# Kernel optimization log

Hardware: AMD Instinct MI355X
Metric: run time of the kernel (lower is better)

Reference implementation:

```python
import jax, jax.numpy as jnp
import numpy as np

B, N, D, S, H, ITERS = 128, 4096, 64, 7, 128, 3
EPS = 1e-8
LN_EPS = 1e-5


def _ln(x, g, b):
    mu = jnp.mean(x, axis=-1, keepdims=True)
    var = jnp.mean(jnp.square(x - mu), axis=-1, keepdims=True)
    return (x - mu) * jax.lax.rsqrt(var + LN_EPS) * g + b


def setup_inputs() -> dict:
    key = jax.random.key(0)
    ks = jax.random.split(key, 20)
    xav = lambda k, shp: jax.random.normal(k, shp, jnp.float32) * (2.0 / sum(shp[-2:])) ** 0.5
    inp = {
        "inputs": jax.random.normal(ks[0], (B, N, D), jnp.float32),
        "noise_bg": jax.random.normal(ks[1], (B, 1, D), jnp.float32),
        "noise_fg": jax.random.normal(ks[2], (B, S - 1, D), jnp.float32),
        "ln_in_g": jnp.ones((D,), jnp.float32), "ln_in_b": jnp.zeros((D,), jnp.float32),
        "ln_slot_g": jnp.ones((D,), jnp.float32), "ln_slot_b": jnp.zeros((D,), jnp.float32),
        "ln_mlp_g": jnp.ones((D,), jnp.float32), "ln_mlp_b": jnp.zeros((D,), jnp.float32),
        "Wq": xav(ks[3], (D, D)), "Wk": xav(ks[4], (D, D)), "Wv": xav(ks[5], (D, D)),
        "W_ih": xav(ks[6], (3 * D, D)), "W_hh": xav(ks[7], (3 * D, D)),
        "b_ih": jnp.zeros((3 * D,), jnp.float32), "b_hh": jnp.zeros((3 * D,), jnp.float32),
        "mlp_w1": xav(ks[8], (H, D)), "mlp_b1": jnp.zeros((H,), jnp.float32),
        "mlp_w2": xav(ks[9], (D, H)), "mlp_b2": jnp.zeros((D,), jnp.float32),
        "slots_bg_mu": xav(ks[10], (1, 1, D)),
        "slots_bg_log_sigma": xav(ks[11], (1, 1, D)),
        "slots_mu": xav(ks[12], (1, 1, D)),
        "slots_log_sigma": xav(ks[13], (1, 1, D)),
    }
    return inp


def _gru(x, h, W_ih, W_hh, b_ih, b_hh):
    # x, h: [M, D]; PyTorch GRUCell math, gate order r, z, n
    gi = x @ W_ih.T + b_ih
    gh = h @ W_hh.T + b_hh
    i_r, i_z, i_n = jnp.split(gi, 3, axis=-1)
    h_r, h_z, h_n = jnp.split(gh, 3, axis=-1)
    r = jax.nn.sigmoid(i_r + h_r)
    z = jax.nn.sigmoid(i_z + h_z)
    n = jnp.tanh(i_n + r * h_n)
    return (1.0 - z) * n + z * h


def reference(inputs, noise_bg, noise_fg, ln_in_g, ln_in_b, ln_slot_g, ln_slot_b,
              ln_mlp_g, ln_mlp_b, Wq, Wk, Wv, W_ih, W_hh, b_ih, b_hh,
              mlp_w1, mlp_b1, mlp_w2, mlp_b2,
              slots_bg_mu, slots_bg_log_sigma, slots_mu, slots_log_sigma):
    x = _ln(inputs, ln_in_g, ln_in_b)          # [B, N, D]
    k = jnp.einsum('bnd,ed->bne', x, Wk)       # [B, N, D]
    v = jnp.einsum('bnd,ed->bne', x, Wv)

    bg = slots_bg_mu + jnp.exp(slots_bg_log_sigma) * noise_bg   # [B, 1, D]
    fg = slots_mu + jnp.exp(slots_log_sigma) * noise_fg          # [B, S-1, D]
    slots = jnp.concatenate([bg, fg], axis=1)                    # [B, S, D]

    scale = D ** (-0.5)
    for _ in range(ITERS):
        slots_prev = slots
        s = _ln(slots, ln_slot_g, ln_slot_b)
        q = jnp.einsum('bsd,ed->bse', s, Wq)                     # [B, S, D]
        logits = scale * jnp.einsum('bnd,bsd->bns', k, q)        # [B, N, S]
        attn = jax.nn.softmax(logits, axis=-1) + EPS             # softmax over slots
        attn = attn / jnp.sum(attn, axis=1, keepdims=True)       # renorm over inputs
        updates = jnp.einsum('bns,bnd->bsd', attn, v)            # [B, S, D]
        h = _gru(updates.reshape(B * S, D), slots_prev.reshape(B * S, D),
                 W_ih, W_hh, b_ih, b_hh).reshape(B, S, D)
        m = _ln(h, ln_mlp_g, ln_mlp_b)
        m = jax.nn.relu(m @ mlp_w1.T + mlp_b1) @ mlp_w2.T + mlp_b2
        slots = h + m
    return slots
```

## Files before the change

kernel.cpp:

```cpp
#include <hip/hip_runtime.h>

#define BB 128
#define NN 4096
#define DD 64
#define SS 7
#define HH 128
#define N_ITERS 3
#define EPS_ATTN 1e-8f
#define LN_EPS 1e-5f

typedef unsigned short ushortT;
using short8  = __attribute__((ext_vector_type(8))) short;
using floatx4 = __attribute__((ext_vector_type(4))) float;
using uint4v  = __attribute__((ext_vector_type(4))) unsigned;

__device__ __forceinline__ float bf2f(unsigned u) {
    return __builtin_bit_cast(float, (u & 0xffffu) << 16);
}
__device__ __forceinline__ ushortT f2bf(float f) {
    unsigned x = __builtin_bit_cast(unsigned, f);
    x = x + 0x7fff + ((x >> 16) & 1);
    return (ushortT)(x >> 16);
}
__device__ __forceinline__ void wave_stats64(float x, float& mu, float& var) {
    float s1 = x, s2 = x * x;
#pragma unroll
    for (int off = 32; off > 0; off >>= 1) {
        s1 += __shfl_xor(s1, off);
        s2 += __shfl_xor(s2, off);
    }
    mu  = s1 * (1.f / 64.f);
    var = s2 * (1.f / 64.f) - mu * mu;
}

__global__ void prep_w(const float* __restrict__ Wih, const float* __restrict__ Whh,
                       const float* __restrict__ w1, const float* __restrict__ w2,
                       const float* __restrict__ Wv, const float* __restrict__ Wq,
                       float* __restrict__ WihT, float* __restrict__ WhhT,
                       float* __restrict__ w1T, float* __restrict__ w2T,
                       float* __restrict__ WvT, float* __restrict__ WqT) {
    int i = blockIdx.x * 256 + threadIdx.x;
    if (i < 12288) {
        int e = i >> 6, d = i & 63;
        WihT[d * 192 + e] = Wih[i];
    } else if (i < 24576) {
        int j = i - 12288; int e = j >> 6, d = j & 63;
        WhhT[d * 192 + e] = Whh[j];
    } else if (i < 32768) {
        int j = i - 24576; int e = j >> 6, d = j & 63;
        w1T[d * 128 + e] = w1[j];
    } else if (i < 40960) {
        int j = i - 32768; int e = j >> 7, h = j & 127;
        w2T[h * 64 + e] = w2[j];
    } else if (i < 45056) {
        int j = i - 40960; int d = j >> 6, e = j & 63;
        WvT[e * 64 + d] = Wv[j];
    } else if (i < 49152) {
        int j = i - 45056; int d = j >> 6, e = j & 63;
        WqT[j] = Wq[e * 64 + d];
    }
}

__global__ __launch_bounds__(256) void attn_kernel(
    int first,
    const float* __restrict__ x,
    const float* __restrict__ lng, const float* __restrict__ lnb,
    ushortT* __restrict__ xnf,
    const float* __restrict__ qkT,
    float* __restrict__ pxn_p, float* __restrict__ den_p) {
    int t = threadIdx.x;
    int ck = blockIdx.x, b = ck >> 5;
    int w = t >> 6, lane = t & 63, m = lane & 15, qd = lane >> 4;
    __shared__ float   qk_lds[512];
    __shared__ ushortT xnT[64 * 140];
    __shared__ ushortT p_lds[16][136];
    __shared__ float   den_w[4][8];

    for (int i = t; i < 512; i += 256) qk_lds[i] = qkT[b * 512 + i];

    unsigned xw[2][8];
    if (first) {
        float4 g4[2][2], b4[2][2];
#pragma unroll
        for (int c = 0; c < 2; ++c) {
            g4[c][0] = *reinterpret_cast<const float4*>(lng + c * 32 + qd * 8);
            g4[c][1] = *reinterpret_cast<const float4*>(lng + c * 32 + qd * 8 + 4);
            b4[c][0] = *reinterpret_cast<const float4*>(lnb + c * 32 + qd * 8);
            b4[c][1] = *reinterpret_cast<const float4*>(lnb + c * 32 + qd * 8 + 4);
        }
#pragma unroll
        for (int tile = 0; tile < 2; ++tile) {
            long R = (long)ck * 128 + w * 32 + tile * 16 + m;
            float4 xa[2][2];
#pragma unroll
            for (int c = 0; c < 2; ++c) {
                xa[c][0] = *reinterpret_cast<const float4*>(x + R * 64 + c * 32 + qd * 8);
                xa[c][1] = *reinterpret_cast<const float4*>(x + R * 64 + c * 32 + qd * 8 + 4);
            }
            float s1 = 0.f, s2 = 0.f;
#pragma unroll
            for (int c = 0; c < 2; ++c)
#pragma unroll
                for (int h = 0; h < 2; ++h) {
                    float4 v = xa[c][h];
                    s1 += v.x + v.y + v.z + v.w;
                    s2 += v.x * v.x + v.y * v.y + v.z * v.z + v.w * v.w;
                }
            s1 += __shfl_xor(s1, 16); s2 += __shfl_xor(s2, 16);
            s1 += __shfl_xor(s1, 32); s2 += __shfl_xor(s2, 32);
            float mu = s1 * (1.f / 64.f);
            float var = s2 * (1.f / 64.f) - mu * mu;
            float rs = rsqrtf(var + LN_EPS);
#pragma unroll
            for (int c = 0; c < 2; ++c)
#pragma unroll
                for (int h = 0; h < 2; ++h) {
                    float n0 = (xa[c][h].x - mu) * rs * g4[c][h].x + b4[c][h].x;
                    float n1 = (xa[c][h].y - mu) * rs * g4[c][h].y + b4[c][h].y;
                    float n2 = (xa[c][h].z - mu) * rs * g4[c][h].z + b4[c][h].z;
                    float n3 = (xa[c][h].w - mu) * rs * g4[c][h].w + b4[c][h].w;
                    xw[tile][c * 4 + h * 2]     = (unsigned)f2bf(n0) | ((unsigned)f2bf(n1) << 16);
                    xw[tile][c * 4 + h * 2 + 1] = (unsigned)f2bf(n2) | ((unsigned)f2bf(n3) << 16);
                }
            ushortT* xp = xnf + (long)ck * 8192 + w * 2048 + tile * 1024 + lane * 16;
            *reinterpret_cast<uint4*>(xp) =
                make_uint4(xw[tile][0], xw[tile][1], xw[tile][2], xw[tile][3]);
            *reinterpret_cast<uint4*>(xp + 8) =
                make_uint4(xw[tile][4], xw[tile][5], xw[tile][6], xw[tile][7]);
        }
    } else {
#pragma unroll
        for (int tile = 0; tile < 2; ++tile) {
            const ushortT* xp = xnf + (long)ck * 8192 + w * 2048 + tile * 1024 + lane * 16;
            uint4 u0 = *reinterpret_cast<const uint4*>(xp);
            uint4 u1 = *reinterpret_cast<const uint4*>(xp + 8);
            xw[tile][0] = u0.x; xw[tile][1] = u0.y; xw[tile][2] = u0.z; xw[tile][3] = u0.w;
            xw[tile][4] = u1.x; xw[tile][5] = u1.y; xw[tile][6] = u1.z; xw[tile][7] = u1.w;
        }
    }
    __syncthreads();

    short8 aq[2];
#pragma unroll
    for (int c = 0; c < 2; ++c) {
        short8 a = {};
        if (m < 8) {
#pragma unroll
            for (int j = 0; j < 8; ++j)
                a[j] = (short)f2bf(qk_lds[(c * 32 + qd * 8 + j) * 8 + m]);
        }
        aq[c] = a;
    }

    float dreg03[4] = {0.f, 0.f, 0.f, 0.f};
    float dreg46[3] = {0.f, 0.f, 0.f};
#pragma unroll
    for (int tile = 0; tile < 2; ++tile) {
        int row = w * 32 + tile * 16 + m;
#pragma unroll
        for (int c = 0; c < 2; ++c)
#pragma unroll
            for (int j = 0; j < 8; ++j) {
                int e = c * 32 + qd * 8 + j;
                xnT[e * 140 + row] =
                    (ushortT)(xw[tile][c * 4 + (j >> 1)] >> ((j & 1) * 16));
            }
        uint4v b0 = {xw[tile][0], xw[tile][1], xw[tile][2], xw[tile][3]};
        uint4v b1 = {xw[tile][4], xw[tile][5], xw[tile][6], xw[tile][7]};
        floatx4 acc = (floatx4){0.f, 0.f, 0.f, 0.f};
        acc = __builtin_amdgcn_mfma_f32_16x16x32_bf16(aq[0],
                  __builtin_bit_cast(short8, b0), acc, 0, 0, 0);
        acc = __builtin_amdgcn_mfma_f32_16x16x32_bf16(aq[1],
                  __builtin_bit_cast(short8, b1), acc, 0, 0, 0);
        float own[4], par[4];
#pragma unroll
        for (int r = 0; r < 4; ++r) { own[r] = acc[r]; par[r] = __shfl_xor(acc[r], 16); }
        float lgA[4], lgB[4];
#pragma unroll
        for (int r = 0; r < 4; ++r) {
            lgA[r] = (qd & 1) ? par[r] : own[r];
            lgB[r] = (qd & 1) ? own[r] : par[r];
        }
        float mx = fmaxf(fmaxf(fmaxf(lgA[0], lgA[1]), fmaxf(lgA[2], lgA[3])),
                         fmaxf(fmaxf(lgB[0], lgB[1]), lgB[2]));
        float eA[4], eB[3], sum = 0.f;
#pragma unroll
        for (int r = 0; r < 4; ++r) { eA[r] = __expf(lgA[r] - mx); sum += eA[r]; }
#pragma unroll
        for (int r = 0; r < 3; ++r) { eB[r] = __expf(lgB[r] - mx); sum += eB[r]; }
        float inv = 1.f / sum;
        if (qd == 0) {
#pragma unroll
            for (int r = 0; r < 4; ++r) {
                ushortT pb = f2bf(eA[r] * inv + EPS_ATTN);
                p_lds[r][row] = pb;
                dreg03[r] += bf2f(pb);
            }
        } else if (qd == 1) {
#pragma unroll
            for (int r = 0; r < 3; ++r) {
                ushortT pb = f2bf(eB[r] * inv + EPS_ATTN);
                p_lds[4 + r][row] = pb;
                dreg46[r] += bf2f(pb);
            }
        }
    }
#pragma unroll
    for (int off = 1; off < 16; off <<= 1) {
#pragma unroll
        for (int r = 0; r < 4; ++r) dreg03[r] += __shfl_xor(dreg03[r], off);
#pragma unroll
        for (int r = 0; r < 3; ++r) dreg46[r] += __shfl_xor(dreg46[r], off);
    }
    if (m == 0 && qd == 0) {
#pragma unroll
        for (int r = 0; r < 4; ++r) den_w[w][r] = dreg03[r];
    } else if (m == 0 && qd == 1) {
#pragma unroll
        for (int r = 0; r < 3; ++r) den_w[w][4 + r] = dreg46[r];
    }
    __syncthreads();

    floatx4 acc2 = (floatx4){0.f, 0.f, 0.f, 0.f};
#pragma unroll
    for (int ks = 0; ks < 4; ++ks) {
        short8 ap = *reinterpret_cast<const short8*>(&p_lds[m][ks * 32 + qd * 8]);
        const ushortT* xp = xnT + (w * 16 + m) * 140 + ks * 32 + qd * 8;
        uint2 u0 = *reinterpret_cast<const uint2*>(xp);
        uint2 u1 = *reinterpret_cast<const uint2*>(xp + 4);
        uint4v bb = {u0.x, u0.y, u1.x, u1.y};
        acc2 = __builtin_amdgcn_mfma_f32_16x16x32_bf16(ap,
                   __builtin_bit_cast(short8, bb), acc2, 0, 0, 0);
    }
#pragma unroll
    for (int r = 0; r < 4; ++r) {
        int s = qd * 4 + r;
        if (s < 7) pxn_p[((long)ck * 7 + s) * 64 + w * 16 + m] = acc2[r];
    }
    if (t < 7) den_p[ck * 8 + t] = den_w[0][t] + den_w[1][t] + den_w[2][t] + den_w[3][t];
}

__global__ __launch_bounds__(192) void slot_update_q(
    int mode,
    const float* __restrict__ pxn_p, const float* __restrict__ den_p,
    float* __restrict__ slots,
    const float* __restrict__ nbg, const float* __restrict__ nfg,
    const float* __restrict__ bgmu, const float* __restrict__ bgls,
    const float* __restrict__ fmu, const float* __restrict__ fls,
    const float* __restrict__ WihT, const float* __restrict__ WhhT,
    const float* __restrict__ bih, const float* __restrict__ bhh,
    const float* __restrict__ lng, const float* __restrict__ lnb,
    const float* __restrict__ w1T, const float* __restrict__ b1,
    const float* __restrict__ w2T, const float* __restrict__ b2,
    const float* __restrict__ WvT, const float* __restrict__ WqT,
    const float* __restrict__ Wk,
    const float* __restrict__ sg, const float* __restrict__ sb,
    float* __restrict__ qkT, float* __restrict__ outp) {
    int bs = blockIdx.x, t = threadIdx.x;
    int b = bs / 7, s = bs % 7;
    __shared__ float pxnL[64], hprevL[64], updL[64], giL[192], ghL[192],
                     mnL[64], m1L[128], xnL[64], qL[64];
    float res = 0.f, dsum = 0.f;
    if (mode == 0) {
        if (t < 64) {
            if (s == 0) res = bgmu[t] + __expf(bgls[t]) * nbg[b * 64 + t];
            else        res = fmu[t]  + __expf(fls[t])  * nfg[(b * 6 + s - 1) * 64 + t];
        }
    } else {
        if (t < 64) {
            float psum = 0.f;
#pragma unroll 8
            for (int c = 0; c < 32; ++c) {
                psum += pxn_p[((long)(b * 32 + c) * 7 + s) * 64 + t];
                dsum += den_p[(b * 32 + c) * 8 + s];
            }
            pxnL[t]   = psum;
            hprevL[t] = slots[bs * 64 + t];
        }
        __syncthreads();
        if (t < 64) {
            float nm = 0.f;
#pragma unroll 8
            for (int e = 0; e < 64; ++e) nm += pxnL[e] * WvT[e * 64 + t];
            updL[t] = nm / dsum;
        }
        __syncthreads();
        {
            float a = bih[t], h2 = bhh[t];
#pragma unroll 8
            for (int d = 0; d < 64; ++d) {
                a  += updL[d]   * WihT[d * 192 + t];
                h2 += hprevL[d] * WhhT[d * 192 + t];
            }
            giL[t] = a; ghL[t] = h2;
        }
        __syncthreads();
        if (t < 64) {
            float r = 1.f / (1.f + __expf(-(giL[t] + ghL[t])));
            float z = 1.f / (1.f + __expf(-(giL[64 + t] + ghL[64 + t])));
            float n = tanhf(giL[128 + t] + r * ghL[128 + t]);
            float h = (1.f - z) * n + z * hprevL[t];
            res = h;
            float mu, var;
            wave_stats64(h, mu, var);
            mnL[t] = (h - mu) * rsqrtf(var + LN_EPS) * lng[t] + lnb[t];
        }
        __syncthreads();
        if (t < 128) {
            float a = b1[t];
#pragma unroll 8
            for (int d = 0; d < 64; ++d) a += mnL[d] * w1T[d * 128 + t];
            m1L[t] = fmaxf(a, 0.f);
        }
        __syncthreads();
        if (t < 64) {
            float a = b2[t];
#pragma unroll 8
            for (int h2 = 0; h2 < 128; ++h2) a += m1L[h2] * w2T[h2 * 64 + t];
            res += a;
        }
    }
    if (t < 64) slots[bs * 64 + t] = res;
    if (mode == 2) {
        if (t < 64) outp[bs * 64 + t] = res;
        return;
    }
    if (t < 64) {
        float mu, var;
        wave_stats64(res, mu, var);
        xnL[t] = (res - mu) * rsqrtf(var + LN_EPS) * sg[t] + sb[t];
    }
    __syncthreads();
    if (t < 64) {
        float q = 0.f;
#pragma unroll 8
        for (int d = 0; d < 64; ++d) q += xnL[d] * WqT[d * 64 + t];
        qL[t] = q * 0.125f;
    }
    __syncthreads();
    if (t < 64) {
        float qk = 0.f;
#pragma unroll 8
        for (int e = 0; e < 64; ++e) qk += qL[e] * Wk[e * 64 + t];
        qkT[b * 512 + t * 8 + s] = qk;
        if (s == 0) qkT[b * 512 + t * 8 + 7] = 0.f;
    }
}

extern "C" void kernel_launch(void* const* d_in, const int* in_sizes, int n_in,
                              void* d_out, int out_size, void* d_ws, size_t ws_size,
                              hipStream_t stream) {
    const float* inputs    = (const float*)d_in[0];
    const float* noise_bg  = (const float*)d_in[1];
    const float* noise_fg  = (const float*)d_in[2];
    const float* ln_in_g   = (const float*)d_in[3];
    const float* ln_in_b   = (const float*)d_in[4];
    const float* ln_slot_g = (const float*)d_in[5];
    const float* ln_slot_b = (const float*)d_in[6];
    const float* ln_mlp_g  = (const float*)d_in[7];
    const float* ln_mlp_b  = (const float*)d_in[8];
    const float* Wq        = (const float*)d_in[9];
    const float* Wk        = (const float*)d_in[10];
    const float* Wv        = (const float*)d_in[11];
    const float* W_ih      = (const float*)d_in[12];
    const float* W_hh      = (const float*)d_in[13];
    const float* b_ih      = (const float*)d_in[14];
    const float* b_hh      = (const float*)d_in[15];
    const float* mlp_w1    = (const float*)d_in[16];
    const float* mlp_b1    = (const float*)d_in[17];
    const float* mlp_w2    = (const float*)d_in[18];
    const float* mlp_b2    = (const float*)d_in[19];
    const float* sbg_mu    = (const float*)d_in[20];
    const float* sbg_ls    = (const float*)d_in[21];
    const float* s_mu      = (const float*)d_in[22];
    const float* s_ls      = (const float*)d_in[23];

    char* ws = (char*)d_ws;
    size_t off = 0;
    auto alloc = [&](size_t bytes) {
        void* p = ws + off;
        off += (bytes + 255) & ~(size_t)255;
        return p;
    };
    ushortT* xnf   = (ushortT*)alloc((size_t)BB * NN * 64 * 2);
    float* slots   = (float*)alloc(57344 * 4);
    float* qkT     = (float*)alloc((size_t)BB * 512 * 4);
    float* pxn_p   = (float*)alloc((size_t)4096 * 7 * 64 * 4);
    float* den_p   = (float*)alloc(4096 * 8 * 4);
    float* WihT    = (float*)alloc(12288 * 4);
    float* WhhT    = (float*)alloc(12288 * 4);
    float* w1T     = (float*)alloc(8192 * 4);
    float* w2T     = (float*)alloc(8192 * 4);
    float* WvT     = (float*)alloc(4096 * 4);
    float* WqT     = (float*)alloc(4096 * 4);
    if (off > ws_size) return;

    prep_w<<<192, 256, 0, stream>>>(W_ih, W_hh, mlp_w1, mlp_w2, Wv, Wq,
                                    WihT, WhhT, w1T, w2T, WvT, WqT);
    slot_update_q<<<896, 192, 0, stream>>>(0, pxn_p, den_p, slots,
                                           noise_bg, noise_fg, sbg_mu, sbg_ls,
                                           s_mu, s_ls, WihT, WhhT, b_ih, b_hh,
                                           ln_mlp_g, ln_mlp_b, w1T, mlp_b1,
                                           w2T, mlp_b2, WvT, WqT, Wk,
                                           ln_slot_g, ln_slot_b,
                                           qkT, (float*)d_out);
    for (int it = 0; it < N_ITERS; ++it) {
        attn_kernel<<<4096, 256, 0, stream>>>((it == 0) ? 1 : 0,
                                              inputs, ln_in_g, ln_in_b,
                                              xnf, qkT, pxn_p, den_p);
        slot_update_q<<<896, 192, 0, stream>>>((it == N_ITERS - 1) ? 2 : 1,
                                               pxn_p, den_p, slots,
                                               noise_bg, noise_fg, sbg_mu, sbg_ls,
                                               s_mu, s_ls, WihT, WhhT, b_ih, b_hh,
                                               ln_mlp_g, ln_mlp_b, w1T, mlp_b1,
                                               w2T, mlp_b2, WvT, WqT, Wk,
                                               ln_slot_g, ln_slot_b,
                                               qkT, (float*)d_out);
    }
}
```

Before: 357.4 us.

## Precombine Wq·Wk, precast qk to bf16, compute attention denominators via MFMA

Folds Wq and Wk into one 64x64 matrix in the prep kernel, so the slot kernel does a single matvec and writes qk directly as bf16 in the layout the attention kernel consumes. The attention kernel loads its MFMA A operands straight from global memory, packs two rows at a time for the transposed LDS writes, runs both tiles' MFMAs together and does softmax once per lane. Column sums for the renormalisation come from an extra MFMA against a ones vector instead of shuffle reductions, which removes one __syncthreads. The slot kernel also reduces den_p in parallel using a separate group of threads. The combined Wq·Wk matrix and the bf16 cast change rounding slightly.

```diff
diff --git a/kernel.cpp b/kernel.cpp
--- a/kernel.cpp
+++ b/kernel.cpp
@@ -14,9 +14,6 @@
 using floatx4 = __attribute__((ext_vector_type(4))) float;
 using uint4v  = __attribute__((ext_vector_type(4))) unsigned;
 
-__device__ __forceinline__ float bf2f(unsigned u) {
-    return __builtin_bit_cast(float, (u & 0xffffu) << 16);
-}
 __device__ __forceinline__ ushortT f2bf(float f) {
     unsigned x = __builtin_bit_cast(unsigned, f);
     x = x + 0x7fff + ((x >> 16) & 1);
@@ -36,9 +33,19 @@
 __global__ void prep_w(const float* __restrict__ Wih, const float* __restrict__ Whh,
                        const float* __restrict__ w1, const float* __restrict__ w2,
                        const float* __restrict__ Wv, const float* __restrict__ Wq,
+                       const float* __restrict__ Wk,
                        float* __restrict__ WihT, float* __restrict__ WhhT,
                        float* __restrict__ w1T, float* __restrict__ w2T,
-                       float* __restrict__ WvT, float* __restrict__ WqT) {
+                       float* __restrict__ WvT, float* __restrict__ WqkT) {
+    if (blockIdx.x >= 192) {
+        int idx = (blockIdx.x - 192) * 256 + threadIdx.x;
+        int d = idx >> 6, tt = idx & 63;
+        float acc = 0.f;
+#pragma unroll 8
+        for (int e = 0; e < 64; ++e) acc += Wk[e * 64 + tt] * Wq[e * 64 + d];
+        WqkT[d * 64 + tt] = 0.125f * acc;
+        return;
+    }
     int i = blockIdx.x * 256 + threadIdx.x;
     if (i < 12288) {
         int e = i >> 6, d = i & 63;
@@ -55,9 +62,6 @@
     } else if (i < 45056) {
         int j = i - 40960; int d = j >> 6, e = j & 63;
         WvT[e * 64 + d] = Wv[j];
-    } else if (i < 49152) {
-        int j = i - 45056; int d = j >> 6, e = j & 63;
-        WqT[j] = Wq[e * 64 + d];
     }
 }
 
@@ -66,17 +70,20 @@
     const float* __restrict__ x,
     const float* __restrict__ lng, const float* __restrict__ lnb,
     ushortT* __restrict__ xnf,
-    const float* __restrict__ qkT,
+    const ushortT* __restrict__ qk_bf,
     float* __restrict__ pxn_p, float* __restrict__ den_p) {
     int t = threadIdx.x;
     int ck = blockIdx.x, b = ck >> 5;
     int w = t >> 6, lane = t & 63, m = lane & 15, qd = lane >> 4;
-    __shared__ float   qk_lds[512];
-    __shared__ ushortT xnT[64 * 140];
-    __shared__ ushortT p_lds[16][136];
-    __shared__ float   den_w[4][8];
-
-    for (int i = t; i < 512; i += 256) qk_lds[i] = qkT[b * 512 + i];
+    __shared__ __align__(16) ushortT xnT[64 * 140];
+    __shared__ __align__(16) ushortT p_lds[16][136];
+
+    short8 aq0 = {}, aq1 = {};
+    if (m < 8) {
+        const ushortT* qb = qk_bf + b * 512 + m * 64 + qd * 8;
+        aq0 = *reinterpret_cast<const short8*>(qb);
+        aq1 = *reinterpret_cast<const short8*>(qb + 32);
+    }
 
     unsigned xw[2][8];
     if (first) {
@@ -138,90 +145,78 @@
             xw[tile][4] = u1.x; xw[tile][5] = u1.y; xw[tile][6] = u1.z; xw[tile][7] = u1.w;
         }
     }
+
+#pragma unroll
+    for (int tile = 0; tile < 2; ++tile) {
+        int Re = (w * 32 + tile * 16 + m) & ~1;
+#pragma unroll
+        for (int c = 0; c < 2; ++c) {
+            unsigned pt[4];
+#pragma unroll
+            for (int k = 0; k < 4; ++k) pt[k] = __shfl_xor(xw[tile][c * 4 + k], 1);
+#pragma unroll
+            for (int kk = 0; kk < 2; ++kk) {
+                unsigned own = (m & 1) ? xw[tile][c * 4 + 2 + kk] : xw[tile][c * 4 + kk];
+                unsigned par = (m & 1) ? pt[2 + kk] : pt[kk];
+                unsigned a   = (m & 1) ? par : own;
+                unsigned bb  = (m & 1) ? own : par;
+                unsigned lo = (a & 0xffffu) | (bb << 16);
+                unsigned hi = (a >> 16)     | (bb & 0xffff0000u);
+                int e = c * 32 + qd * 8 + 2 * kk + ((m & 1) ? 4 : 0);
+                *reinterpret_cast<unsigned*>(&xnT[e * 140 + Re])       = lo;
+                *reinterpret_cast<unsigned*>(&xnT[(e + 1) * 140 + Re]) = hi;
+            }
+        }
+    }
+
+    floatx4 accT0 = {0.f, 0.f, 0.f, 0.f}, accT1 = {0.f, 0.f, 0.f, 0.f};
+    {
+        uint4v b00 = {xw[0][0], xw[0][1], xw[0][2], xw[0][3]};
+        uint4v b01 = {xw[0][4], xw[0][5], xw[0][6], xw[0][7]};
+        accT0 = __builtin_amdgcn_mfma_f32_16x16x32_bf16(aq0,
+                    __builtin_bit_cast(short8, b00), accT0, 0, 0, 0);
+        accT0 = __builtin_amdgcn_mfma_f32_16x16x32_bf16(aq1,
+                    __builtin_bit_cast(short8, b01), accT0, 0, 0, 0);
+        uint4v b10 = {xw[1][0], xw[1][1], xw[1][2], xw[1][3]};
+        uint4v b11 = {xw[1][4], xw[1][5], xw[1][6], xw[1][7]};
+        accT1 = __builtin_amdgcn_mfma_f32_16x16x32_bf16(aq0,
+                    __builtin_bit_cast(short8, b10), accT1, 0, 0, 0);
+        accT1 = __builtin_amdgcn_mfma_f32_16x16x32_bf16(aq1,
+                    __builtin_bit_cast(short8, b11), accT1, 0, 0, 0);
+    }
+
+    float lgA[4], lgB[4];
+#pragma unroll
+    for (int r = 0; r < 4; ++r) {
+        float hi = __shfl_xor(accT1[r], 32);
+        float wk = (qd < 2) ? accT0[r] : hi;
+        float pr = __shfl_xor(wk, 16);
+        lgA[r] = (qd & 1) ? pr : wk;
+        lgB[r] = (qd & 1) ? wk : pr;
+    }
+    float mx = fmaxf(fmaxf(fmaxf(lgA[0], lgA[1]), fmaxf(lgA[2], lgA[3])),
+                     fmaxf(fmaxf(lgB[0], lgB[1]), lgB[2]));
+    float eA[4], eB[3], sum = 0.f;
+#pragma unroll
+    for (int r = 0; r < 4; ++r) { eA[r] = __expf(lgA[r] - mx); sum += eA[r]; }
+#pragma unroll
+    for (int r = 0; r < 3; ++r) { eB[r] = __expf(lgB[r] - mx); sum += eB[r]; }
+    float inv = 1.f / sum;
+    int prow = w * 32 + (qd >> 1) * 16 + m;
+    if ((qd & 1) == 0) {
+#pragma unroll
+        for (int r = 0; r < 4; ++r) p_lds[r][prow] = f2bf(eA[r] * inv + EPS_ATTN);
+    } else {
+#pragma unroll
+        for (int r = 0; r < 3; ++r) p_lds[4 + r][prow] = f2bf(eB[r] * inv + EPS_ATTN);
+    }
     __syncthreads();
 
-    short8 aq[2];
-#pragma unroll
-    for (int c = 0; c < 2; ++c) {
-        short8 a = {};
-        if (m < 8) {
-#pragma unroll
-            for (int j = 0; j < 8; ++j)
-                a[j] = (short)f2bf(qk_lds[(c * 32 + qd * 8 + j) * 8 + m]);
-        }
-        aq[c] = a;
-    }
-
-    float dreg03[4] = {0.f, 0.f, 0.f, 0.f};
-    float dreg46[3] = {0.f, 0.f, 0.f};
-#pragma unroll
-    for (int tile = 0; tile < 2; ++tile) {
-        int row = w * 32 + tile * 16 + m;
-#pragma unroll
-        for (int c = 0; c < 2; ++c)
-#pragma unroll
-            for (int j = 0; j < 8; ++j) {
-                int e = c * 32 + qd * 8 + j;
-                xnT[e * 140 + row] =
-                    (ushortT)(xw[tile][c * 4 + (j >> 1)] >> ((j & 1) * 16));
-            }
-        uint4v b0 = {xw[tile][0], xw[tile][1], xw[tile][2], xw[tile][3]};
-        uint4v b1 = {xw[tile][4], xw[tile][5], xw[tile][6], xw[tile][7]};
-        floatx4 acc = (floatx4){0.f, 0.f, 0.f, 0.f};
-        acc = __builtin_amdgcn_mfma_f32_16x16x32_bf16(aq[0],
-                  __builtin_bit_cast(short8, b0), acc, 0, 0, 0);
-        acc = __builtin_amdgcn_mfma_f32_16x16x32_bf16(aq[1],
-                  __builtin_bit_cast(short8, b1), acc, 0, 0, 0);
-        float own[4], par[4];
-#pragma unroll
-        for (int r = 0; r < 4; ++r) { own[r] = acc[r]; par[r] = __shfl_xor(acc[r], 16); }
-        float lgA[4], lgB[4];
-#pragma unroll
-        for (int r = 0; r < 4; ++r) {
-            lgA[r] = (qd & 1) ? par[r] : own[r];
-            lgB[r] = (qd & 1) ? own[r] : par[r];
-        }
-        float mx = fmaxf(fmaxf(fmaxf(lgA[0], lgA[1]), fmaxf(lgA[2], lgA[3])),
-                         fmaxf(fmaxf(lgB[0], lgB[1]), lgB[2]));
-        float eA[4], eB[3], sum = 0.f;
-#pragma unroll
-        for (int r = 0; r < 4; ++r) { eA[r] = __expf(lgA[r] - mx); sum += eA[r]; }
-#pragma unroll
-        for (int r = 0; r < 3; ++r) { eB[r] = __expf(lgB[r] - mx); sum += eB[r]; }
-        float inv = 1.f / sum;
-        if (qd == 0) {
-#pragma unroll
-            for (int r = 0; r < 4; ++r) {
-                ushortT pb = f2bf(eA[r] * inv + EPS_ATTN);
-                p_lds[r][row] = pb;
-                dreg03[r] += bf2f(pb);
-            }
-        } else if (qd == 1) {
-#pragma unroll
-            for (int r = 0; r < 3; ++r) {
-                ushortT pb = f2bf(eB[r] * inv + EPS_ATTN);
-                p_lds[4 + r][row] = pb;
-                dreg46[r] += bf2f(pb);
-            }
-        }
-    }
-#pragma unroll
-    for (int off = 1; off < 16; off <<= 1) {
-#pragma unroll
-        for (int r = 0; r < 4; ++r) dreg03[r] += __shfl_xor(dreg03[r], off);
-#pragma unroll
-        for (int r = 0; r < 3; ++r) dreg46[r] += __shfl_xor(dreg46[r], off);
-    }
-    if (m == 0 && qd == 0) {
-#pragma unroll
-        for (int r = 0; r < 4; ++r) den_w[w][r] = dreg03[r];
-    } else if (m == 0 && qd == 1) {
-#pragma unroll
-        for (int r = 0; r < 3; ++r) den_w[w][4 + r] = dreg46[r];
-    }
-    __syncthreads();
-
-    floatx4 acc2 = (floatx4){0.f, 0.f, 0.f, 0.f};
+    short8 ones;
+#pragma unroll
+    for (int j = 0; j < 8; ++j) ones[j] = (short)0x3F80;
+
+    floatx4 acc2 = {0.f, 0.f, 0.f, 0.f}, accd = {0.f, 0.f, 0.f, 0.f};
 #pragma unroll
     for (int ks = 0; ks < 4; ++ks) {
         short8 ap = *reinterpret_cast<const short8*>(&p_lds[m][ks * 32 + qd * 8]);
@@ -231,13 +226,20 @@
         uint4v bb = {u0.x, u0.y, u1.x, u1.y};
         acc2 = __builtin_amdgcn_mfma_f32_16x16x32_bf16(ap,
                    __builtin_bit_cast(short8, bb), acc2, 0, 0, 0);
+        accd = __builtin_amdgcn_mfma_f32_16x16x32_bf16(ap, ones, accd, 0, 0, 0);
     }
 #pragma unroll
     for (int r = 0; r < 4; ++r) {
         int s = qd * 4 + r;
         if (s < 7) pxn_p[((long)ck * 7 + s) * 64 + w * 16 + m] = acc2[r];
     }
-    if (t < 7) den_p[ck * 8 + t] = den_w[0][t] + den_w[1][t] + den_w[2][t] + den_w[3][t];
+    if (w == 0 && m == 0) {
+#pragma unroll
+        for (int r = 0; r < 4; ++r) {
+            int s = qd * 4 + r;
+            if (s < 7) den_p[ck * 8 + s] = accd[r];
+        }
+    }
 }
 
 __global__ __launch_bounds__(192) void slot_update_q(
@@ -252,15 +254,15 @@
     const float* __restrict__ lng, const float* __restrict__ lnb,
     const float* __restrict__ w1T, const float* __restrict__ b1,
     const float* __restrict__ w2T, const float* __restrict__ b2,
-    const float* __restrict__ WvT, const float* __restrict__ WqT,
-    const float* __restrict__ Wk,
+    const float* __restrict__ WvT, const float* __restrict__ WqkT,
     const float* __restrict__ sg, const float* __restrict__ sb,
-    float* __restrict__ qkT, float* __restrict__ outp) {
+    ushortT* __restrict__ qk_bf, float* __restrict__ outp) {
     int bs = blockIdx.x, t = threadIdx.x;
     int b = bs / 7, s = bs % 7;
     __shared__ float pxnL[64], hprevL[64], updL[64], giL[192], ghL[192],
-                     mnL[64], m1L[128], xnL[64], qL[64];
-    float res = 0.f, dsum = 0.f;
+                     mnL[64], m1L[128], xnL[64];
+    __shared__ float denL;
+    float res = 0.f;
     if (mode == 0) {
         if (t < 64) {
             if (s == 0) res = bgmu[t] + __expf(bgls[t]) * nbg[b * 64 + t];
@@ -270,19 +272,23 @@
         if (t < 64) {
             float psum = 0.f;
 #pragma unroll 8
-            for (int c = 0; c < 32; ++c) {
+            for (int c = 0; c < 32; ++c)
                 psum += pxn_p[((long)(b * 32 + c) * 7 + s) * 64 + t];
-                dsum += den_p[(b * 32 + c) * 8 + s];
-            }
-            pxnL[t]   = psum;
-            hprevL[t] = slots[bs * 64 + t];
+            pxnL[t] = psum;
+        } else if (t < 96) {
+            float dv = den_p[(b * 32 + (t - 64)) * 8 + s];
+#pragma unroll
+            for (int off = 16; off > 0; off >>= 1) dv += __shfl_xor(dv, off, 32);
+            if (t == 64) denL = dv;
+        } else if (t >= 128) {
+            hprevL[t - 128] = slots[bs * 64 + (t - 128)];
         }
         __syncthreads();
         if (t < 64) {
             float nm = 0.f;
 #pragma unroll 8
             for (int e = 0; e < 64; ++e) nm += pxnL[e] * WvT[e * 64 + t];
-            updL[t] = nm / dsum;
+            updL[t] = nm / denL;
         }
         __syncthreads();
         {
@@ -332,18 +338,11 @@
     }
     __syncthreads();
     if (t < 64) {
-        float q = 0.f;
-#pragma unroll 8
-        for (int d = 0; d < 64; ++d) q += xnL[d] * WqT[d * 64 + t];
-        qL[t] = q * 0.125f;
-    }
-    __syncthreads();
-    if (t < 64) {
         float qk = 0.f;
 #pragma unroll 8
-        for (int e = 0; e < 64; ++e) qk += qL[e] * Wk[e * 64 + t];
-        qkT[b * 512 + t * 8 + s] = qk;
-        if (s == 0) qkT[b * 512 + t * 8 + 7] = 0.f;
+        for (int d = 0; d < 64; ++d) qk += xnL[d] * WqkT[d * 64 + t];
+        qk_bf[b * 512 + s * 64 + t] = f2bf(qk);
+        if (s == 0) qk_bf[b * 512 + 7 * 64 + t] = 0;
     }
 }
 
@@ -384,7 +383,7 @@
     };
     ushortT* xnf   = (ushortT*)alloc((size_t)BB * NN * 64 * 2);
     float* slots   = (float*)alloc(57344 * 4);
-    float* qkT     = (float*)alloc((size_t)BB * 512 * 4);
+    ushortT* qk_bf = (ushortT*)alloc((size_t)BB * 512 * 2);
     float* pxn_p   = (float*)alloc((size_t)4096 * 7 * 64 * 4);
     float* den_p   = (float*)alloc(4096 * 8 * 4);
     float* WihT    = (float*)alloc(12288 * 4);
@@ -392,29 +391,29 @@
     float* w1T     = (float*)alloc(8192 * 4);
     float* w2T     = (float*)alloc(8192 * 4);
     float* WvT     = (float*)alloc(4096 * 4);
-    float* WqT     = (float*)alloc(4096 * 4);
+    float* WqkT    = (float*)alloc(4096 * 4);
     if (off > ws_size) return;
 
-    prep_w<<<192, 256, 0, stream>>>(W_ih, W_hh, mlp_w1, mlp_w2, Wv, Wq,
-                                    WihT, WhhT, w1T, w2T, WvT, WqT);
+    prep_w<<<208, 256, 0, stream>>>(W_ih, W_hh, mlp_w1, mlp_w2, Wv, Wq, Wk,
+                                    WihT, WhhT, w1T, w2T, WvT, WqkT);
     slot_update_q<<<896, 192, 0, stream>>>(0, pxn_p, den_p, slots,
                                            noise_bg, noise_fg, sbg_mu, sbg_ls,
                                            s_mu, s_ls, WihT, WhhT, b_ih, b_hh,
                                            ln_mlp_g, ln_mlp_b, w1T, mlp_b1,
-                                           w2T, mlp_b2, WvT, WqT, Wk,
+                                           w2T, mlp_b2, WvT, WqkT,
                                            ln_slot_g, ln_slot_b,
-                                           qkT, (float*)d_out);
+                                           qk_bf, (float*)d_out);
     for (int it = 0; it < N_ITERS; ++it) {
         attn_kernel<<<4096, 256, 0, stream>>>((it == 0) ? 1 : 0,
                                               inputs, ln_in_g, ln_in_b,
-                                              xnf, qkT, pxn_p, den_p);
+                                              xnf, qk_bf, pxn_p, den_p);
         slot_update_q<<<896, 192, 0, stream>>>((it == N_ITERS - 1) ? 2 : 1,
                                                pxn_p, den_p, slots,
                                                noise_bg, noise_fg, sbg_mu, sbg_ls,
                                                s_mu, s_ls, WihT, WhhT, b_ih, b_hh,
                                                ln_mlp_g, ln_mlp_b, w1T, mlp_b1,
-                                               w2T, mlp_b2, WvT, WqT, Wk,
+                                               w2T, mlp_b2, WvT, WqkT,
                                                ln_slot_g, ln_slot_b,
-                                               qkT, (float*)d_out);
-    }
-}
+                                               qk_bf, (float*)d_out);
+    }
+}
```

Measured after the change: 352.9 us. Within noise of the previous version (-1.3%).
